# Optimization experiments

Measured on AMD Instinct MI355X. Metric: run time of the kernel, lower is better.

The kernel has to match this reference:

```python
import jax, jax.numpy as jnp
import numpy as np
from jax import lax

T, B, IN, H = 512, 64, 1024, 1024
N_LAYER = 2


def _kaiming_uniform(key, shape):
    # torch kaiming_uniform_ default: a=sqrt(5) -> gain = sqrt(2/(1+5)) = 1/sqrt(3)
    fan_in = shape[1]
    gain = 1.0 / np.sqrt(3.0)
    bound = gain * np.sqrt(3.0 / fan_in)
    return jax.random.uniform(key, shape, jnp.float32, -bound, bound)


def setup_inputs() -> dict:
    key = jax.random.key(0)
    ks = jax.random.split(key, 5)
    inputs = jax.random.normal(ks[0], (T, B, IN), jnp.float32)
    # layer 0: input_size -> hidden; layer 1: hidden -> hidden
    w_ih0 = _kaiming_uniform(ks[1], (4 * H, IN))
    w_hh0 = _kaiming_uniform(ks[2], (4 * H, H))
    b0 = jnp.zeros((4 * H,), jnp.float32)
    w_ih1 = _kaiming_uniform(ks[3], (4 * H, H))
    w_hh1 = _kaiming_uniform(ks[4], (4 * H, H))
    b1 = jnp.zeros((4 * H,), jnp.float32)
    return {"inputs": inputs, "w_ih0": w_ih0, "w_hh0": w_hh0, "b0": b0,
            "w_ih1": w_ih1, "w_hh1": w_hh1, "b1": b1}


def _lstm_layer(x_seq, w_ih, w_hh, b):
    # x_seq: [T, B, D]; initial h = ones (per source hx=None branch), c = zeros
    batch = x_seq.shape[1]
    hidden = w_hh.shape[1]
    h0 = jnp.ones((batch, hidden), x_seq.dtype)
    c0 = jnp.zeros((batch, hidden), x_seq.dtype)

    def step(carry, x_t):
        h, c = carry
        gates = x_t @ w_ih.T + h @ w_hh.T + b  # [B, 4H]
        i, f, g, o = jnp.split(gates, 4, axis=-1)
        i = jax.nn.sigmoid(i)
        f = jax.nn.sigmoid(f)
        g = jnp.tanh(g)
        o = jax.nn.sigmoid(o)
        c_new = f * c + i * g
        h_new = o * jnp.tanh(c_new)
        return (h_new, c_new), h_new

    _, hs = lax.scan(step, (h0, c0), x_seq)
    return hs  # [T, B, H]


def reference(inputs, w_ih0, w_hh0, b0, w_ih1, w_hh1, b1):
    h1 = _lstm_layer(inputs, w_ih0, w_hh0, b0)
    h2 = _lstm_layer(h1, w_ih1, w_hh1, b1)
    return h2  # [T, B, H]
```

## Files before the change

### kernel.cpp

```cpp
#include <hip/hip_runtime.h>
#include <cstdint>
#include <cstddef>


typedef _Float16 f16;
typedef _Float16 f16x8 __attribute__((ext_vector_type(8)));
typedef _Float16 f16x4 __attribute__((ext_vector_type(4)));
typedef float    f32x4 __attribute__((ext_vector_type(4)));
typedef unsigned long long u64;

#define T_STEPS 512
#define BH      65536
#define NBLK    192

static const size_t OFF_FLAG = 0;
static const size_t OFF_H2   = 0x1000;
static const size_t OFF_H1   = 0x90000;

__global__ void prep_kernel(f16* __restrict__ h1, unsigned* __restrict__ flags)
{
    const int NONES = BH / 4;
    const int NZ    = 256 / 4;
    int tid    = blockIdx.x * blockDim.x + threadIdx.x;
    int stride = gridDim.x * blockDim.x;
    f16x4 one = { (f16)1.f, (f16)1.f, (f16)1.f, (f16)1.f };
    uint4 z = { 0u, 0u, 0u, 0u };
    for (int i = tid; i < NONES + NZ; i += stride) {
        if (i < NONES) ((f16x4*)h1)[i] = one;
        else           ((uint4*)flags)[i - NONES] = z;
    }
}

__device__ __forceinline__ float sigm(float x) { return 1.f/(1.f + __expf(-x)); }
__device__ __forceinline__ float tanh_f(float x) {
    float e = __expf(-2.f*fabsf(x));
    float r = (1.f - e)/(1.f + e);
    return x >= 0.f ? r : -r;
}
__device__ __forceinline__ f16x8 cvt8(float4 a, float4 b) {
    f16x8 r;
    r[0]=(f16)a.x; r[1]=(f16)a.y; r[2]=(f16)a.z; r[3]=(f16)a.w;
    r[4]=(f16)b.x; r[5]=(f16)b.y; r[6]=(f16)b.z; r[7]=(f16)b.w;
    return r;
}

__device__ __forceinline__ unsigned poll1(const unsigned* p) {
    unsigned r;
    asm volatile("global_load_dword %0, %1, off sc1\n\ts_waitcnt vmcnt(0)"
                 : "=v"(r) : "v"(p) : "memory");
    return r;
}
__device__ __forceinline__ void flag_store(unsigned* p, unsigned v) {
    asm volatile("global_store_dword %0, %1, off sc1" :: "v"(p), "v"(v) : "memory");
}
__device__ __forceinline__ f16x8 ald16(const f16* p) {
    union { u64 q[2]; f16x8 v; } u;
    u.q[0] = __hip_atomic_load((const u64*)p,       __ATOMIC_RELAXED, __HIP_MEMORY_SCOPE_AGENT);
    u.q[1] = __hip_atomic_load((const u64*)(p + 4), __ATOMIC_RELAXED, __HIP_MEMORY_SCOPE_AGENT);
    return u.v;
}

__global__ __launch_bounds__(512, 2)
void lstm_kernel(const float* __restrict__ x,
                 const float* __restrict__ wih0, const float* __restrict__ whh0,
                 const float* __restrict__ b0,
                 const float* __restrict__ wih1, const float* __restrict__ whh1,
                 const float* __restrict__ b1,
                 f16* __restrict__ h1, f16* __restrict__ h2,
                 float* __restrict__ out, unsigned* __restrict__ flags)
{
    __shared__ float lds_part[32768];
    __shared__ float lds_out[4096];

    const int tid   = threadIdx.x;
    const int bid   = blockIdx.x;
    const int wave  = tid >> 6, lane = tid & 63;
    const int l15   = lane & 15, l4 = lane >> 4;
    const f32x4 zz = { 0.f, 0.f, 0.f, 0.f };

    if (bid < 128) {
        const int bg = bid >> 6, jg = bid & 63, j0 = jg << 4;
        const int kq = wave;

        f16x8 Bf[32];
        f32x4 acc[8];
        {
            const float* wsrc = (kq < 4) ? wih0 : whh0;
            const int kp = (kq & 3) * 256;
#pragma unroll
            for (int nt = 0; nt < 4; nt++) {
                const float* rp = wsrc + (size_t)(nt*1024 + j0 + l15)*1024 + kp + l4*8;
#pragma unroll
                for (int kc = 0; kc < 8; kc++) {
                    float4 a = *(const float4*)(rp + kc*32);
                    float4 b = *(const float4*)(rp + kc*32 + 4);
                    Bf[nt*8 + kc] = cvt8(a, b);
                }
            }
#pragma unroll
            for (int i = 0; i < 32; i++) asm volatile("" : "+v"(Bf[i]));
        }

        const int u  = ((tid >> 8) << 3) | (tid & 7);
        const int bm = (tid >> 3) & 31;
        const float bi  = b0[j0+u],      bff = b0[1024+j0+u];
        const float bgg = b0[2048+j0+u], boo = b0[3072+j0+u];
        float c = 0.f;
        const int m_ = bm >> 4, r_ = bm & 15;
        const int lanei = ((r_ >> 2) << 4) | u, rr = r_ & 3;

        for (int s = 0; s <= T_STEPS; s++) {
            const bool act = (s < T_STEPS);
            if (act) {
#pragma unroll
                for (int i = 0; i < 8; i++) acc[i] = zz;
                if (kq < 4) {
                    const float* a0 = x + (size_t)s*BH + (size_t)(bg*32 + l15)*1024 + kq*256 + l4*8;
                    const float* a1 = a0 + 16*1024;
#pragma unroll
                    for (int kc = 0; kc < 8; kc++) {
                        f16x8 A0 = cvt8(*(const float4*)(a0 + kc*32), *(const float4*)(a0 + kc*32 + 4));
                        f16x8 A1 = cvt8(*(const float4*)(a1 + kc*32), *(const float4*)(a1 + kc*32 + 4));
#pragma unroll
                        for (int nt = 0; nt < 4; nt++) {
                            acc[nt]   = __builtin_amdgcn_mfma_f32_16x16x32_f16(A0, Bf[nt*8+kc], acc[nt],   0,0,0);
                            acc[4+nt] = __builtin_amdgcn_mfma_f32_16x16x32_f16(A1, Bf[nt*8+kc], acc[4+nt], 0,0,0);
                        }
                    }
                } else {
                    if (s > 0) {
                        const bool mine = (lane < 16);
                        const int  pj   = ((kq - 4) << 4) + l15;
                        const bool skip = (!mine) || (pj == jg);
                        const unsigned* p = flags + bg*64 + (mine ? pj : 0);
                        for (;;) {
                            unsigned v = poll1(p);
                            if (__all(skip || (v >= (unsigned)s))) break;
                            __builtin_amdgcn_s_sleep(2);
                        }
                    }
                    const f16* a0 = h1 + (size_t)s*BH + bg*32768 + ((kq-4)*32 + l4)*256 + l15*8;
                    const f16* a1 = a0 + 128;
#pragma unroll
                    for (int kc = 0; kc < 8; kc++) {
                        f16x8 A0 = *(const f16x8*)(a0 + kc*1024);
                        f16x8 A1 = *(const f16x8*)(a1 + kc*1024);
#pragma unroll
                        for (int nt = 0; nt < 4; nt++) {
                            acc[nt]   = __builtin_amdgcn_mfma_f32_16x16x32_f16(A0, Bf[nt*8+kc], acc[nt],   0,0,0);
                            acc[4+nt] = __builtin_amdgcn_mfma_f32_16x16x32_f16(A1, Bf[nt*8+kc], acc[4+nt], 0,0,0);
                        }
                    }
                }
                const int pb = wave*2048 + lane*4;
#pragma unroll
                for (int i = 0; i < 8; i++)
                    *(f32x4*)&lds_part[pb + i*256] = acc[i];
            }
            __syncthreads();
            if (act) {
                f32x4 sum = *(const f32x4*)&lds_part[tid*4];
#pragma unroll
                for (int q = 1; q < 8; q++)
                    sum += *(const f32x4*)&lds_part[q*2048 + tid*4];
                *(f32x4*)&lds_out[tid*4] = sum;
            }
            __syncthreads();
            if (act) {
                float gi = lds_out[(m_*4+0)*256 + lanei*4 + rr] + bi;
                float gf = lds_out[(m_*4+1)*256 + lanei*4 + rr] + bff;
                float gg = lds_out[(m_*4+2)*256 + lanei*4 + rr] + bgg;
                float go = lds_out[(m_*4+3)*256 + lanei*4 + rr] + boo;
                float iv = sigm(gi), fv = sigm(gf), gv = tanh_f(gg), ov = sigm(go);
                c = fv*c + iv*gv;
                float h = ov * tanh_f(c);
                f16 hv = (f16)h;
                short hs = __builtin_bit_cast(short, hv);
                __hip_atomic_store((short*)(h1 + (size_t)(s+1)*BH + bg*32768 + jg*512 + tid),
                                   hs, __ATOMIC_RELAXED, __HIP_MEMORY_SCOPE_AGENT);
            }
            __builtin_amdgcn_s_waitcnt(0);
            __syncthreads();
            if (tid == 0) flag_store(flags + bid, (unsigned)(s + 1));
        }
    } else {
        const int jg1 = bid - 128, j0 = jg1 << 4;
        const int ks = wave;

        f16x8 Bf[32];
        f32x4 acc[16];
        {
            const float* wsrc = (ks < 4) ? wih1 : whh1;
            const int kp = (ks & 3) * 256;
#pragma unroll
            for (int nt = 0; nt < 4; nt++) {
                const float* rp = wsrc + (size_t)(nt*1024 + j0 + l15)*1024 + kp + l4*8;
#pragma unroll
                for (int kc = 0; kc < 8; kc++) {
                    float4 a = *(const float4*)(rp + kc*32);
                    float4 b = *(const float4*)(rp + kc*32 + 4);
                    Bf[nt*8 + kc] = cvt8(a, b);
                }
            }
#pragma unroll
            for (int i = 0; i < 32; i++) asm volatile("" : "+v"(Bf[i]));
        }

        const int bb = tid >> 3, u0 = tid & 7, u1 = 8 + u0;
        const float bi0 = b1[j0+u0], bf0 = b1[1024+j0+u0], bg0v = b1[2048+j0+u0], bo0 = b1[3072+j0+u0];
        const float bi1 = b1[j0+u1], bf1 = b1[1024+j0+u1], bg1v = b1[2048+j0+u1], bo1 = b1[3072+j0+u1];
        float c0 = 0.f, c1 = 0.f;
        const int mt_ = bb >> 4, r_ = bb & 15, rr = r_ & 3, lb = (r_ >> 2) << 4;

        for (int s = 0; s <= T_STEPS; s++) {
            const bool act = (s >= 1);
            if (act) {
#pragma unroll
                for (int i = 0; i < 16; i++) acc[i] = zz;
                if (ks < 4) {
                    {
                        const bool mine = (lane < 32);
                        const int  pidx = ((lane >> 4) * 64) + (ks << 4) + l15;
                        const unsigned* p = flags + (mine ? pidx : 0);
                        for (;;) {
                            unsigned v = poll1(p);
                            if (__all(!mine || (v >= (unsigned)s))) break;
                            __builtin_amdgcn_s_sleep(2);
                        }
                    }
                    const f16* a0 = h1 + (size_t)s*BH + (ks*32 + l4)*256 + l15*8;
#pragma unroll
                    for (int kc = 0; kc < 8; kc++) {
                        f16x8 A0 = *(const f16x8*)(a0 + kc*1024);
                        f16x8 A1 = *(const f16x8*)(a0 + kc*1024 + 128);
                        f16x8 A2 = *(const f16x8*)(a0 + kc*1024 + 32768);
                        f16x8 A3 = *(const f16x8*)(a0 + kc*1024 + 32768 + 128);
#pragma unroll
                        for (int nt = 0; nt < 4; nt++) {
                            acc[nt]    = __builtin_amdgcn_mfma_f32_16x16x32_f16(A0, Bf[nt*8+kc], acc[nt],    0,0,0);
                            acc[4+nt]  = __builtin_amdgcn_mfma_f32_16x16x32_f16(A1, Bf[nt*8+kc], acc[4+nt],  0,0,0);
                            acc[8+nt]  = __builtin_amdgcn_mfma_f32_16x16x32_f16(A2, Bf[nt*8+kc], acc[8+nt],  0,0,0);
                            acc[12+nt] = __builtin_amdgcn_mfma_f32_16x16x32_f16(A3, Bf[nt*8+kc], acc[12+nt], 0,0,0);
                        }
                    }
                } else if (s == 1) {
                    f16x8 A1s;
#pragma unroll
                    for (int e = 0; e < 8; e++) A1s[e] = (f16)1.f;
#pragma unroll
                    for (int kc = 0; kc < 8; kc++) {
#pragma unroll
                        for (int nt = 0; nt < 4; nt++) {
                            acc[nt]    = __builtin_amdgcn_mfma_f32_16x16x32_f16(A1s, Bf[nt*8+kc], acc[nt],    0,0,0);
                            acc[4+nt]  = __builtin_amdgcn_mfma_f32_16x16x32_f16(A1s, Bf[nt*8+kc], acc[4+nt],  0,0,0);
                            acc[8+nt]  = __builtin_amdgcn_mfma_f32_16x16x32_f16(A1s, Bf[nt*8+kc], acc[8+nt],  0,0,0);
                            acc[12+nt] = __builtin_amdgcn_mfma_f32_16x16x32_f16(A1s, Bf[nt*8+kc], acc[12+nt], 0,0,0);
                        }
                    }
                } else {
                    {
                        const bool mine = (lane < 16);
                        const int  pj   = ((ks - 4) << 4) + l15;
                        const bool skip = (!mine) || (pj == jg1);
                        const unsigned* p = flags + 128 + (mine ? pj : 0);
                        for (;;) {
                            unsigned v = poll1(p);
                            if (__all(skip || (v >= (unsigned)s))) break;
                            __builtin_amdgcn_s_sleep(2);
                        }
                    }
                    const f16* a0 = h2 + (size_t)((s-1) & 3)*BH + ((ks-4)*32 + l4)*512 + l15*8;
#pragma unroll
                    for (int kc = 0; kc < 8; kc++) {
                        f16x8 A0 = ald16(a0 + kc*2048);
                        f16x8 A1 = ald16(a0 + kc*2048 + 128);
                        f16x8 A2 = ald16(a0 + kc*2048 + 256);
                        f16x8 A3 = ald16(a0 + kc*2048 + 384);
#pragma unroll
                        for (int nt = 0; nt < 4; nt++) {
                            acc[nt]    = __builtin_amdgcn_mfma_f32_16x16x32_f16(A0, Bf[nt*8+kc], acc[nt],    0,0,0);
                            acc[4+nt]  = __builtin_amdgcn_mfma_f32_16x16x32_f16(A1, Bf[nt*8+kc], acc[4+nt],  0,0,0);
                            acc[8+nt]  = __builtin_amdgcn_mfma_f32_16x16x32_f16(A2, Bf[nt*8+kc], acc[8+nt],  0,0,0);
                            acc[12+nt] = __builtin_amdgcn_mfma_f32_16x16x32_f16(A3, Bf[nt*8+kc], acc[12+nt], 0,0,0);
                        }
                    }
                }
                const int pb = ks*4096 + lane*4;
#pragma unroll
                for (int i = 0; i < 16; i++)
                    *(f32x4*)&lds_part[pb + i*256] = acc[i];
            }
            __syncthreads();
            if (act) {
#pragma unroll
                for (int g = 0; g < 2; g++) {
                    const int gi_ = tid + g*512;
                    f32x4 sum = *(const f32x4*)&lds_part[gi_*4];
#pragma unroll
                    for (int q = 1; q < 8; q++)
                        sum += *(const f32x4*)&lds_part[q*4096 + gi_*4];
                    *(f32x4*)&lds_out[gi_*4] = sum;
                }
            }
            __syncthreads();
            if (act) {
                float gi0 = lds_out[(mt_*4+0)*256 + (lb+u0)*4 + rr] + bi0;
                float gf0 = lds_out[(mt_*4+1)*256 + (lb+u0)*4 + rr] + bf0;
                float gg0 = lds_out[(mt_*4+2)*256 + (lb+u0)*4 + rr] + bg0v;
                float go0 = lds_out[(mt_*4+3)*256 + (lb+u0)*4 + rr] + bo0;
                float gi1 = lds_out[(mt_*4+0)*256 + (lb+u1)*4 + rr] + bi1;
                float gf1 = lds_out[(mt_*4+1)*256 + (lb+u1)*4 + rr] + bf1;
                float gg1 = lds_out[(mt_*4+2)*256 + (lb+u1)*4 + rr] + bg1v;
                float go1 = lds_out[(mt_*4+3)*256 + (lb+u1)*4 + rr] + bo1;
                float iv0 = sigm(gi0), fv0 = sigm(gf0), gv0 = tanh_f(gg0), ov0 = sigm(go0);
                float iv1 = sigm(gi1), fv1 = sigm(gf1), gv1 = tanh_f(gg1), ov1 = sigm(go1);
                c0 = fv0*c0 + iv0*gv0;
                c1 = fv1*c1 + iv1*gv1;
                float hv0 = ov0 * tanh_f(c0);
                float hv1 = ov1 * tanh_f(c1);
                f16* h2w = h2 + (size_t)(s & 3)*BH;
                short hs0 = __builtin_bit_cast(short, (f16)hv0);
                short hs1 = __builtin_bit_cast(short, (f16)hv1);
                __hip_atomic_store((short*)(h2w + jg1*1024 + tid),       hs0,
                                   __ATOMIC_RELAXED, __HIP_MEMORY_SCOPE_AGENT);
                __hip_atomic_store((short*)(h2w + jg1*1024 + 512 + tid), hs1,
                                   __ATOMIC_RELAXED, __HIP_MEMORY_SCOPE_AGENT);
                out[(size_t)(s-1)*BH + bb*1024 + j0 + u0] = hv0;
                out[(size_t)(s-1)*BH + bb*1024 + j0 + u1] = hv1;
            }
            __builtin_amdgcn_s_waitcnt(0);
            __syncthreads();
            if (tid == 0) flag_store(flags + bid, (unsigned)(s + 1));
        }
    }
}

extern "C" void kernel_launch(void* const* d_in, const int* in_sizes, int n_in,
                              void* d_out, int out_size, void* d_ws, size_t ws_size,
                              hipStream_t stream) {
    const float* x    = (const float*)d_in[0];
    const float* wih0 = (const float*)d_in[1];
    const float* whh0 = (const float*)d_in[2];
    const float* b0   = (const float*)d_in[3];
    const float* wih1 = (const float*)d_in[4];
    const float* whh1 = (const float*)d_in[5];
    const float* b1   = (const float*)d_in[6];
    float* out = (float*)d_out;

    char* ws = (char*)d_ws;
    unsigned* flags = (unsigned*)(ws + OFF_FLAG);
    f16* h2         = (f16*)(ws + OFF_H2);
    f16* h1         = (f16*)(ws + OFF_H1);

    prep_kernel<<<256, 256, 0, stream>>>(h1, flags);
    lstm_kernel<<<NBLK, 512, 0, stream>>>(x, wih0, whh0, b0, wih1, whh1, b1,
                                          h1, h2, out, flags);
}
```

Before: 4.889 ms.

## Split layer-1 blocks by batch halves and store full h2 history

Layer 1 moves from 64 blocks covering the full batch of 64 to 128 blocks, each covering 32 batch rows, so every layer-1 block does half the MFMA work per step and polls only its batch partition's flags. This halves the LDS reduction buffers. When the workspace is large enough, h2 is kept as a full per-step history instead of a 4-slot ring, which allows plain vector loads in place of the paired 64-bit atomic loads. The cost is 256 blocks at 2 per CU, which needs enough CUs to keep every block resident for the spin-waits, plus more workspace memory.

```diff
diff --git a/kernel.cpp b/kernel.cpp
--- a/kernel.cpp
+++ b/kernel.cpp
@@ -11,11 +11,13 @@
 
 #define T_STEPS 512
 #define BH      65536
-#define NBLK    192
-
-static const size_t OFF_FLAG = 0;
-static const size_t OFF_H2   = 0x1000;
-static const size_t OFF_H1   = 0x90000;
+#define NBLK    256
+
+static const size_t OFF_FLAG   = 0;
+static const size_t OFF_H2RING = 0x1000;
+static const size_t OFF_H1     = 0x90000;
+static const size_t OFF_H2BIG  = 0x40B0000;
+static const size_t WS_NEED_BIG = 0x80D0000;
 
 __global__ void prep_kernel(f16* __restrict__ h1, unsigned* __restrict__ flags)
 {
@@ -59,7 +61,12 @@
     u.q[1] = __hip_atomic_load((const u64*)(p + 4), __ATOMIC_RELAXED, __HIP_MEMORY_SCOPE_AGENT);
     return u.v;
 }
-
+template<int HIST> __device__ __forceinline__ f16x8 h2ld(const f16* p) {
+    if constexpr (HIST) return *(const f16x8*)p;
+    else                return ald16(p);
+}
+
+template<int HIST>
 __global__ __launch_bounds__(512, 2)
 void lstm_kernel(const float* __restrict__ x,
                  const float* __restrict__ wih0, const float* __restrict__ whh0,
@@ -69,8 +76,8 @@
                  f16* __restrict__ h1, f16* __restrict__ h2,
                  float* __restrict__ out, unsigned* __restrict__ flags)
 {
-    __shared__ float lds_part[32768];
-    __shared__ float lds_out[4096];
+    __shared__ float lds_part[16384];
+    __shared__ float lds_out[2048];
 
     const int tid   = threadIdx.x;
     const int bid   = blockIdx.x;
@@ -184,11 +191,11 @@
             if (tid == 0) flag_store(flags + bid, (unsigned)(s + 1));
         }
     } else {
-        const int jg1 = bid - 128, j0 = jg1 << 4;
-        const int ks = wave;
+        const int p_  = (bid - 128) >> 6, jg1 = (bid - 128) & 63, j0 = jg1 << 4;
+        const int ks  = wave;
 
         f16x8 Bf[32];
-        f32x4 acc[16];
+        f32x4 acc[8];
         {
             const float* wsrc = (ks < 4) ? wih1 : whh1;
             const int kp = (ks & 3) * 256;
@@ -206,41 +213,40 @@
             for (int i = 0; i < 32; i++) asm volatile("" : "+v"(Bf[i]));
         }
 
-        const int bb = tid >> 3, u0 = tid & 7, u1 = 8 + u0;
-        const float bi0 = b1[j0+u0], bf0 = b1[1024+j0+u0], bg0v = b1[2048+j0+u0], bo0 = b1[3072+j0+u0];
-        const float bi1 = b1[j0+u1], bf1 = b1[1024+j0+u1], bg1v = b1[2048+j0+u1], bo1 = b1[3072+j0+u1];
-        float c0 = 0.f, c1 = 0.f;
-        const int mt_ = bb >> 4, r_ = bb & 15, rr = r_ & 3, lb = (r_ >> 2) << 4;
+        const int u  = ((tid >> 8) << 3) | (tid & 7);
+        const int bm = (tid >> 3) & 31;
+        const float bi  = b1[j0+u],      bff = b1[1024+j0+u];
+        const float bgg = b1[2048+j0+u], boo = b1[3072+j0+u];
+        float c = 0.f;
+        const int m_ = bm >> 4, r_ = bm & 15;
+        const int lanei = ((r_ >> 2) << 4) | u, rr = r_ & 3;
 
         for (int s = 0; s <= T_STEPS; s++) {
             const bool act = (s >= 1);
             if (act) {
 #pragma unroll
-                for (int i = 0; i < 16; i++) acc[i] = zz;
+                for (int i = 0; i < 8; i++) acc[i] = zz;
                 if (ks < 4) {
                     {
-                        const bool mine = (lane < 32);
-                        const int  pidx = ((lane >> 4) * 64) + (ks << 4) + l15;
-                        const unsigned* p = flags + (mine ? pidx : 0);
+                        const bool mine = (lane < 16);
+                        const int  pidx = p_*64 + (ks << 4) + l15;
+                        const unsigned* pp = flags + (mine ? pidx : 0);
                         for (;;) {
-                            unsigned v = poll1(p);
+                            unsigned v = poll1(pp);
                             if (__all(!mine || (v >= (unsigned)s))) break;
                             __builtin_amdgcn_s_sleep(2);
                         }
                     }
-                    const f16* a0 = h1 + (size_t)s*BH + (ks*32 + l4)*256 + l15*8;
+                    const f16* a0 = h1 + (size_t)s*BH + p_*32768 + (ks*32 + l4)*256 + l15*8;
+                    const f16* a1 = a0 + 128;
 #pragma unroll
                     for (int kc = 0; kc < 8; kc++) {
                         f16x8 A0 = *(const f16x8*)(a0 + kc*1024);
-                        f16x8 A1 = *(const f16x8*)(a0 + kc*1024 + 128);
-                        f16x8 A2 = *(const f16x8*)(a0 + kc*1024 + 32768);
-                        f16x8 A3 = *(const f16x8*)(a0 + kc*1024 + 32768 + 128);
-#pragma unroll
-                        for (int nt = 0; nt < 4; nt++) {
-                            acc[nt]    = __builtin_amdgcn_mfma_f32_16x16x32_f16(A0, Bf[nt*8+kc], acc[nt],    0,0,0);
-                            acc[4+nt]  = __builtin_amdgcn_mfma_f32_16x16x32_f16(A1, Bf[nt*8+kc], acc[4+nt],  0,0,0);
-                            acc[8+nt]  = __builtin_amdgcn_mfma_f32_16x16x32_f16(A2, Bf[nt*8+kc], acc[8+nt],  0,0,0);
-                            acc[12+nt] = __builtin_amdgcn_mfma_f32_16x16x32_f16(A3, Bf[nt*8+kc], acc[12+nt], 0,0,0);
+                        f16x8 A1 = *(const f16x8*)(a1 + kc*1024);
+#pragma unroll
+                        for (int nt = 0; nt < 4; nt++) {
+                            acc[nt]   = __builtin_amdgcn_mfma_f32_16x16x32_f16(A0, Bf[nt*8+kc], acc[nt],   0,0,0);
+                            acc[4+nt] = __builtin_amdgcn_mfma_f32_16x16x32_f16(A1, Bf[nt*8+kc], acc[4+nt], 0,0,0);
                         }
                     }
                 } else if (s == 1) {
@@ -251,10 +257,8 @@
                     for (int kc = 0; kc < 8; kc++) {
 #pragma unroll
                         for (int nt = 0; nt < 4; nt++) {
-                            acc[nt]    = __builtin_amdgcn_mfma_f32_16x16x32_f16(A1s, Bf[nt*8+kc], acc[nt],    0,0,0);
-                            acc[4+nt]  = __builtin_amdgcn_mfma_f32_16x16x32_f16(A1s, Bf[nt*8+kc], acc[4+nt],  0,0,0);
-                            acc[8+nt]  = __builtin_amdgcn_mfma_f32_16x16x32_f16(A1s, Bf[nt*8+kc], acc[8+nt],  0,0,0);
-                            acc[12+nt] = __builtin_amdgcn_mfma_f32_16x16x32_f16(A1s, Bf[nt*8+kc], acc[12+nt], 0,0,0);
+                            acc[nt]   = __builtin_amdgcn_mfma_f32_16x16x32_f16(A1s, Bf[nt*8+kc], acc[nt],   0,0,0);
+                            acc[4+nt] = __builtin_amdgcn_mfma_f32_16x16x32_f16(A1s, Bf[nt*8+kc], acc[4+nt], 0,0,0);
                         }
                     }
                 } else {
@@ -262,71 +266,55 @@
                         const bool mine = (lane < 16);
                         const int  pj   = ((ks - 4) << 4) + l15;
                         const bool skip = (!mine) || (pj == jg1);
-                        const unsigned* p = flags + 128 + (mine ? pj : 0);
+                        const unsigned* pp = flags + 128 + p_*64 + (mine ? pj : 0);
                         for (;;) {
-                            unsigned v = poll1(p);
+                            unsigned v = poll1(pp);
                             if (__all(skip || (v >= (unsigned)s))) break;
                             __builtin_amdgcn_s_sleep(2);
                         }
                     }
-                    const f16* a0 = h2 + (size_t)((s-1) & 3)*BH + ((ks-4)*32 + l4)*512 + l15*8;
-#pragma unroll
-                    for (int kc = 0; kc < 8; kc++) {
-                        f16x8 A0 = ald16(a0 + kc*2048);
-                        f16x8 A1 = ald16(a0 + kc*2048 + 128);
-                        f16x8 A2 = ald16(a0 + kc*2048 + 256);
-                        f16x8 A3 = ald16(a0 + kc*2048 + 384);
-#pragma unroll
-                        for (int nt = 0; nt < 4; nt++) {
-                            acc[nt]    = __builtin_amdgcn_mfma_f32_16x16x32_f16(A0, Bf[nt*8+kc], acc[nt],    0,0,0);
-                            acc[4+nt]  = __builtin_amdgcn_mfma_f32_16x16x32_f16(A1, Bf[nt*8+kc], acc[4+nt],  0,0,0);
-                            acc[8+nt]  = __builtin_amdgcn_mfma_f32_16x16x32_f16(A2, Bf[nt*8+kc], acc[8+nt],  0,0,0);
-                            acc[12+nt] = __builtin_amdgcn_mfma_f32_16x16x32_f16(A3, Bf[nt*8+kc], acc[12+nt], 0,0,0);
+                    const size_t slab = HIST ? (size_t)(s - 1) : (size_t)((s - 1) & 3);
+                    const f16* a0 = h2 + slab*BH + p_*32768 + ((ks-4)*32 + l4)*256 + l15*8;
+                    const f16* a1 = a0 + 128;
+#pragma unroll
+                    for (int kc = 0; kc < 8; kc++) {
+                        f16x8 A0 = h2ld<HIST>(a0 + kc*1024);
+                        f16x8 A1 = h2ld<HIST>(a1 + kc*1024);
+#pragma unroll
+                        for (int nt = 0; nt < 4; nt++) {
+                            acc[nt]   = __builtin_amdgcn_mfma_f32_16x16x32_f16(A0, Bf[nt*8+kc], acc[nt],   0,0,0);
+                            acc[4+nt] = __builtin_amdgcn_mfma_f32_16x16x32_f16(A1, Bf[nt*8+kc], acc[4+nt], 0,0,0);
                         }
                     }
                 }
-                const int pb = ks*4096 + lane*4;
-#pragma unroll
-                for (int i = 0; i < 16; i++)
+                const int pb = wave*2048 + lane*4;
+#pragma unroll
+                for (int i = 0; i < 8; i++)
                     *(f32x4*)&lds_part[pb + i*256] = acc[i];
             }
             __syncthreads();
             if (act) {
-#pragma unroll
-                for (int g = 0; g < 2; g++) {
-                    const int gi_ = tid + g*512;
-                    f32x4 sum = *(const f32x4*)&lds_part[gi_*4];
-#pragma unroll
-                    for (int q = 1; q < 8; q++)
-                        sum += *(const f32x4*)&lds_part[q*4096 + gi_*4];
-                    *(f32x4*)&lds_out[gi_*4] = sum;
-                }
-            }
-            __syncthreads();
-            if (act) {
-                float gi0 = lds_out[(mt_*4+0)*256 + (lb+u0)*4 + rr] + bi0;
-                float gf0 = lds_out[(mt_*4+1)*256 + (lb+u0)*4 + rr] + bf0;
-                float gg0 = lds_out[(mt_*4+2)*256 + (lb+u0)*4 + rr] + bg0v;
-                float go0 = lds_out[(mt_*4+3)*256 + (lb+u0)*4 + rr] + bo0;
-                float gi1 = lds_out[(mt_*4+0)*256 + (lb+u1)*4 + rr] + bi1;
-                float gf1 = lds_out[(mt_*4+1)*256 + (lb+u1)*4 + rr] + bf1;
-                float gg1 = lds_out[(mt_*4+2)*256 + (lb+u1)*4 + rr] + bg1v;
-                float go1 = lds_out[(mt_*4+3)*256 + (lb+u1)*4 + rr] + bo1;
-                float iv0 = sigm(gi0), fv0 = sigm(gf0), gv0 = tanh_f(gg0), ov0 = sigm(go0);
-                float iv1 = sigm(gi1), fv1 = sigm(gf1), gv1 = tanh_f(gg1), ov1 = sigm(go1);
-                c0 = fv0*c0 + iv0*gv0;
-                c1 = fv1*c1 + iv1*gv1;
-                float hv0 = ov0 * tanh_f(c0);
-                float hv1 = ov1 * tanh_f(c1);
-                f16* h2w = h2 + (size_t)(s & 3)*BH;
-                short hs0 = __builtin_bit_cast(short, (f16)hv0);
-                short hs1 = __builtin_bit_cast(short, (f16)hv1);
-                __hip_atomic_store((short*)(h2w + jg1*1024 + tid),       hs0,
-                                   __ATOMIC_RELAXED, __HIP_MEMORY_SCOPE_AGENT);
-                __hip_atomic_store((short*)(h2w + jg1*1024 + 512 + tid), hs1,
-                                   __ATOMIC_RELAXED, __HIP_MEMORY_SCOPE_AGENT);
-                out[(size_t)(s-1)*BH + bb*1024 + j0 + u0] = hv0;
-                out[(size_t)(s-1)*BH + bb*1024 + j0 + u1] = hv1;
+                f32x4 sum = *(const f32x4*)&lds_part[tid*4];
+#pragma unroll
+                for (int q = 1; q < 8; q++)
+                    sum += *(const f32x4*)&lds_part[q*2048 + tid*4];
+                *(f32x4*)&lds_out[tid*4] = sum;
+            }
+            __syncthreads();
+            if (act) {
+                float gi = lds_out[(m_*4+0)*256 + lanei*4 + rr] + bi;
+                float gf = lds_out[(m_*4+1)*256 + lanei*4 + rr] + bff;
+                float gg = lds_out[(m_*4+2)*256 + lanei*4 + rr] + bgg;
+                float go = lds_out[(m_*4+3)*256 + lanei*4 + rr] + boo;
+                float iv = sigm(gi), fv = sigm(gf), gv = tanh_f(gg), ov = sigm(go);
+                c = fv*c + iv*gv;
+                float h = ov * tanh_f(c);
+                f16 hv = (f16)h;
+                short hs = __builtin_bit_cast(short, hv);
+                const size_t wslab = HIST ? (size_t)s : (size_t)(s & 3);
+                __hip_atomic_store((short*)(h2 + wslab*BH + p_*32768 + jg1*512 + tid),
+                                   hs, __ATOMIC_RELAXED, __HIP_MEMORY_SCOPE_AGENT);
+                out[(size_t)(s-1)*BH + (size_t)(p_*32 + bm)*1024 + j0 + u] = h;
             }
             __builtin_amdgcn_s_waitcnt(0);
             __syncthreads();
@@ -349,10 +337,15 @@
 
     char* ws = (char*)d_ws;
     unsigned* flags = (unsigned*)(ws + OFF_FLAG);
-    f16* h2         = (f16*)(ws + OFF_H2);
     f16* h1         = (f16*)(ws + OFF_H1);
+    const bool big  = (ws_size >= WS_NEED_BIG);
+    f16* h2         = (f16*)(ws + (big ? OFF_H2BIG : OFF_H2RING));
 
     prep_kernel<<<256, 256, 0, stream>>>(h1, flags);
-    lstm_kernel<<<NBLK, 512, 0, stream>>>(x, wih0, whh0, b0, wih1, whh1, b1,
-                                          h1, h2, out, flags);
-}
+    if (big)
+        lstm_kernel<1><<<NBLK, 512, 0, stream>>>(x, wih0, whh0, b0, wih1, whh1, b1,
+                                                 h1, h2, out, flags);
+    else
+        lstm_kernel<0><<<NBLK, 512, 0, stream>>>(x, wih0, whh0, b0, wih1, whh1, b1,
+                                                 h1, h2, out, flags);
+}
```

Measured after the change: 5.646 ms. +15.5%, slower.
